# Optimization experiments

Hardware: AMD Instinct MI355X
Metric: run time of the kernel (lower is better)

## Reference

```python
import jax, jax.numpy as jnp
import numpy as np

B, D, H, L = 131072, 128, 128, 4
LN_EPS = 1e-5


def _layernorm(x, gamma, beta):
    mu = jnp.mean(x, axis=-1, keepdims=True)
    var = jnp.mean(jnp.square(x - mu), axis=-1, keepdims=True)
    return (x - mu) * jax.lax.rsqrt(var + LN_EPS) * gamma + beta


def setup_inputs() -> dict:
    key = jax.random.key(0)
    ks = jax.random.split(key, 12)
    t = jax.random.uniform(ks[0], (1,), dtype=jnp.float32)
    p = jax.random.normal(ks[1], (B, D), dtype=jnp.float32)
    w = jax.random.normal(ks[2], (B, D), dtype=jnp.float32)
    # VectorField parameters (torch default inits approximated with scaled normals)
    W_in = jax.random.normal(ks[3], (H, D), dtype=jnp.float32) * (1.0 / np.sqrt(D))
    b_in = jax.random.normal(ks[4], (H,), dtype=jnp.float32) * 0.01
    # FourierFeature buffers, scale=1.0 (hard-coded in VectorField)
    fw = jax.random.normal(ks[5], (L, H), dtype=jnp.float32) * 1.0
    fb = jax.random.uniform(ks[6], (L, H), dtype=jnp.float32) * 1.0
    gamma = jnp.ones((L, H), dtype=jnp.float32)
    beta = jnp.zeros((L, H), dtype=jnp.float32)
    Wl = jax.random.normal(ks[7], (L, H, H), dtype=jnp.float32) * (1.0 / np.sqrt(H))
    bl = jax.random.normal(ks[8], (L, H), dtype=jnp.float32) * 0.01
    W_out = jax.random.normal(ks[9], (D, H), dtype=jnp.float32) * (1.0 / np.sqrt(H))
    b_out = jax.random.normal(ks[10], (D,), dtype=jnp.float32) * 0.01
    return {"t": t, "p": p, "w": w, "W_in": W_in, "b_in": b_in, "fw": fw,
            "fb": fb, "gamma": gamma, "beta": beta, "Wl": Wl, "bl": bl,
            "W_out": W_out, "b_out": b_out}


def reference(t, p, w, W_in, b_in, fw, fb, gamma, beta, Wl, bl, W_out, b_out):
    # VectorField.forward: all ops act per-row, so batched vjp == vmapped per-sample vjp
    def vf(pp):  # pp: [B, D]
        h = pp @ W_in.T + b_in                      # [B, H]
        for i in range(L):
            h = h + jnp.sin(t * fw[i] + fb[i])      # time embedding, broadcast [H]
            h = jax.nn.softplus(h)
            h = _layernorm(h, gamma[i], beta[i])
            h = h @ Wl[i].T + bl[i]
        return h @ W_out.T + b_out                  # [B, D]

    dp, vjp_fn = jax.vjp(vf, p)
    dw = -vjp_fn(w)[0]
    return dp, dw
```

## Files before the change

kernel.cpp:

```cpp
#include <hip/hip_runtime.h>

typedef unsigned short u16;
typedef unsigned int   u32;
typedef __attribute__((ext_vector_type(8))) short bf16x8;
typedef __attribute__((ext_vector_type(4))) float f32x4;

#define NB 131072
#define LN_EPS 1e-5f
#define EX_STRIDE 136

__device__ __forceinline__ u16 f2b(float f){
  union { __bf16 h; u16 u; } c; c.h = (__bf16)f; return c.u;
}
__device__ __forceinline__ float upk(u32 pr, int hi){
  union { u32 u; float f; } c; c.u = hi ? (pr & 0xFFFF0000u) : (pr << 16); return c.f;
}
__device__ __forceinline__ float rowsum16(float x){
  x += __shfl_xor(x, 1);
  x += __shfl_xor(x, 2);
  x += __shfl_xor(x, 4);
  x += __shfl_xor(x, 8);
  return x;
}
__device__ __forceinline__ bf16x8 cvt8(const float* __restrict__ s){
  f32x4 x0 = *(const f32x4*)s;
  f32x4 x1 = *(const f32x4*)(s + 4);
  bf16x8 r;
  r[0]=(short)f2b(x0[0]); r[1]=(short)f2b(x0[1]);
  r[2]=(short)f2b(x0[2]); r[3]=(short)f2b(x0[3]);
  r[4]=(short)f2b(x1[0]); r[5]=(short)f2b(x1[1]);
  r[6]=(short)f2b(x1[2]); r[7]=(short)f2b(x1[3]);
  return r;
}

__device__ __forceinline__ void glds16(const u16* g, u16* l){
  __builtin_amdgcn_global_load_lds(
      (const __attribute__((address_space(1))) void*)g,
      (__attribute__((address_space(3))) void*)l, 16, 0, 0);
}
__device__ __forceinline__ void stageB(const u16* __restrict__ packB, int m,
                                       u16* __restrict__ bst, int wave, int lane){
  const u16* src = packB + m*16384 + wave*512 + lane*8;
  u16*       dst = bst   + wave*512;
  #pragma unroll
  for (int k = 0; k < 8; k++)
    glds16(src + k*2048, dst + k*2048);
}

__device__ __forceinline__ void gemm16(const bf16x8 a[4], const u16* __restrict__ Blds,
                                       int lane, f32x4 C[8]){
  const bf16x8* Bf = (const bf16x8*)Blds;
  #pragma unroll
  for (int nt = 0; nt < 8; nt++){
    f32x4 c = {0.f, 0.f, 0.f, 0.f};
    #pragma unroll
    for (int kt = 0; kt < 4; kt++){
      bf16x8 b = Bf[(nt*4 + kt)*64 + lane];
      c = __builtin_amdgcn_mfma_f32_16x16x32_bf16(a[kt], b, c, 0, 0, 0);
    }
    C[nt] = c;
  }
}

__global__ void prep_kernel(const float* __restrict__ t,   const float* __restrict__ W_in,
                            const float* __restrict__ b_in,const float* __restrict__ fw,
                            const float* __restrict__ fb,  const float* __restrict__ gamma,
                            const float* __restrict__ beta,const float* __restrict__ Wl,
                            const float* __restrict__ bl,  const float* __restrict__ W_out,
                            const float* __restrict__ b_out,
                            u16* __restrict__ packB, float* __restrict__ vecs)
{
  int bid = blockIdx.x, tid = threadIdx.x;
  if (bid < 768){
    int e    = bid*256 + tid;
    int m    = e >> 14;
    int r    = e & 16383;
    int fi   = r >> 9;
    int lane = (r >> 3) & 63;
    int j    = r & 7;
    int nt = fi >> 2, kt = fi & 3;
    int k = kt*32 + (lane >> 4)*8 + j;
    int n = nt*16 + (lane & 15);
    const float* src; bool tr;
    if      (m == 0){ src = W_in;              tr = true;  }
    else if (m <= 4){ src = Wl + (m-1)*16384;  tr = true;  }
    else if (m == 5){ src = W_out;             tr = true;  }
    else if (m == 6){ src = W_out;             tr = false; }
    else if (m <=10){ src = Wl + (m-7)*16384;  tr = false; }
    else            { src = W_in;              tr = false; }
    packB[e] = f2b(tr ? src[n*128 + k] : src[k*128 + n]);
  } else {
    int idx = (bid - 768)*256 + tid;
    float tv = t[0];
    float v;
    if      (idx <  512) v = sinf(tv * fw[idx] + fb[idx]);
    else if (idx <  640) v = b_in[idx - 512];
    else if (idx < 1152) v = bl[idx - 640];
    else if (idx < 1664) v = gamma[idx - 1152];
    else if (idx < 2176) v = beta[idx - 1664];
    else                 v = b_out[idx - 2176];
    vecs[idx] = v;
  }
}

__global__ __launch_bounds__(256, 3)
void fused_vf(const float* __restrict__ p, const float* __restrict__ w,
              const u16* __restrict__ packB, const float* __restrict__ vecs,
              float* __restrict__ dp_out, float* __restrict__ dw_out)
{
  __shared__ __align__(16) u16  exch[4 * 16 * EX_STRIDE];
  __shared__ __align__(16) u16  bstage[16384];

  const int tid  = threadIdx.x;
  const int wave = tid >> 6, lane = tid & 63;
  const int l15  = lane & 15, quad = lane >> 4;
  u16* ex = exch + wave * 16 * EX_STRIDE;

  stageB(packB, 0, bstage, wave, lane);
  const float* sS    = vecs;
  const float* sBin  = vecs + 512;
  const float* sBl   = vecs + 640;
  const float* sGam  = vecs + 1152;
  const float* sBet  = vecs + 1664;
  const float* sBout = vecs + 2176;

  const long rowBase = (long)blockIdx.x * 64 + wave * 16;

  u32   sp_ck[4][8][2];
  float mus[4][4];
  float invs[4][4];

  bf16x8 a[4];
  f32x4  C[8];

  {
    const float* pr = p + (size_t)(rowBase + l15)*128 + quad*8;
    #pragma unroll
    for (int kt = 0; kt < 4; kt++) a[kt] = cvt8(pr + kt*32);
  }
  __syncthreads();
  gemm16(a, bstage, lane, C);
  #pragma unroll
  for (int nt = 0; nt < 8; nt++){
    float bv = sBin[nt*16 + l15];
    #pragma unroll
    for (int r = 0; r < 4; r++) C[nt][r] += bv;
  }

  #pragma unroll
  for (int i = 0; i < 4; i++){
    __syncthreads();
    stageB(packB, 1+i, bstage, wave, lane);
    float sum[4] = {0,0,0,0}, ssq[4] = {0,0,0,0};
    #pragma unroll
    for (int nt = 0; nt < 8; nt++){
      float se = sS[i*128 + nt*16 + l15];
      #pragma unroll
      for (int r = 0; r < 4; r++){
        float x  = C[nt][r] + se;
        float e  = __expf(-fabsf(x));
        float li = __logf(1.0f + e);
        float sp = fmaxf(x, 0.0f) + li;
        u16 sb = f2b(sp);
        if (r & 1) sp_ck[i][nt][r>>1] |= ((u32)sb) << 16; else sp_ck[i][nt][r>>1] = sb;
        sum[r] += sp; ssq[r] += sp*sp;
        C[nt][r] = sp;
      }
    }
    float mu[4], inv[4];
    #pragma unroll
    for (int r = 0; r < 4; r++){
      float m1 = rowsum16(sum[r]) * (1.0f/128.0f);
      float m2 = rowsum16(ssq[r]) * (1.0f/128.0f);
      float var = m2 - m1*m1;
      mu[r] = m1; inv[r] = rsqrtf(fmaxf(var, 0.0f) + LN_EPS);
      mus[i][r] = m1; invs[i][r] = inv[r];
    }
    #pragma unroll
    for (int nt = 0; nt < 8; nt++){
      float g_ = sGam[i*128 + nt*16 + l15];
      float b_ = sBet[i*128 + nt*16 + l15];
      #pragma unroll
      for (int r = 0; r < 4; r++){
        float xh = (C[nt][r] - mu[r]) * inv[r];
        float v = xh * g_ + b_;
        ex[(quad*4 + r)*EX_STRIDE + nt*16 + l15] = f2b(v);
      }
    }
    __syncthreads();
    {
      const u16* rp = ex + l15*EX_STRIDE + quad*8;
      #pragma unroll
      for (int kt = 0; kt < 4; kt++) a[kt] = *(const bf16x8*)(rp + kt*32);
    }
    gemm16(a, bstage, lane, C);
    #pragma unroll
    for (int nt = 0; nt < 8; nt++){
      float bv = sBl[i*128 + nt*16 + l15];
      #pragma unroll
      for (int r = 0; r < 4; r++) C[nt][r] += bv;
    }
  }

  __syncthreads();
  stageB(packB, 5, bstage, wave, lane);
  #pragma unroll
  for (int nt = 0; nt < 8; nt++)
    #pragma unroll
    for (int r = 0; r < 4; r++)
      ex[(quad*4 + r)*EX_STRIDE + nt*16 + l15] = f2b(C[nt][r]);
  __syncthreads();
  {
    const u16* rp = ex + l15*EX_STRIDE + quad*8;
    #pragma unroll
    for (int kt = 0; kt < 4; kt++) a[kt] = *(const bf16x8*)(rp + kt*32);
  }
  gemm16(a, bstage, lane, C);
  {
    float* gp = dp_out + (size_t)rowBase*128;
    #pragma unroll
    for (int nt = 0; nt < 8; nt++){
      float bv = sBout[nt*16 + l15];
      #pragma unroll
      for (int r = 0; r < 4; r++)
        gp[(size_t)(quad*4 + r)*128 + nt*16 + l15] = C[nt][r] + bv;
    }
  }

  __syncthreads();
  stageB(packB, 6, bstage, wave, lane);
  {
    const float* wr = w + (size_t)(rowBase + l15)*128 + quad*8;
    #pragma unroll
    for (int kt = 0; kt < 4; kt++) a[kt] = cvt8(wr + kt*32);
  }
  __syncthreads();
  gemm16(a, bstage, lane, C);
  __syncthreads();
  stageB(packB, 10, bstage, wave, lane);

  #pragma unroll
  for (int ii = 0; ii < 4; ii++){
    const int i = 3 - ii;
    #pragma unroll
    for (int nt = 0; nt < 8; nt++)
      #pragma unroll
      for (int r = 0; r < 4; r++)
        ex[(quad*4 + r)*EX_STRIDE + nt*16 + l15] = f2b(C[nt][r]);
    __syncthreads();
    {
      const u16* rp = ex + l15*EX_STRIDE + quad*8;
      #pragma unroll
      for (int kt = 0; kt < 4; kt++) a[kt] = *(const bf16x8*)(rp + kt*32);
    }
    gemm16(a, bstage, lane, C);
    __syncthreads();
    stageB(packB, (ii < 3) ? (7 + (2 - ii)) : 11, bstage, wave, lane);
    float s1[4] = {0,0,0,0}, s2[4] = {0,0,0,0};
    #pragma unroll
    for (int nt = 0; nt < 8; nt++){
      float g_ = sGam[i*128 + nt*16 + l15];
      #pragma unroll
      for (int r = 0; r < 4; r++){
        float sp = upk(sp_ck[i][nt][r>>1], r & 1);
        float xh = (sp - mus[i][r]) * invs[i][r];
        float gx = C[nt][r] * g_;
        s1[r] += gx; s2[r] += gx * xh;
        C[nt][r] = gx;
      }
    }
    float m1[4], m2[4];
    #pragma unroll
    for (int r = 0; r < 4; r++){
      m1[r] = rowsum16(s1[r]) * (1.0f/128.0f);
      m2[r] = rowsum16(s2[r]) * (1.0f/128.0f);
    }
    #pragma unroll
    for (int nt = 0; nt < 8; nt++)
      #pragma unroll
      for (int r = 0; r < 4; r++){
        float sp = upk(sp_ck[i][nt][r>>1], r & 1);
        float xh = (sp - mus[i][r]) * invs[i][r];
        float sg = 1.0f - __expf(-sp);
        float gu = invs[i][r] * (C[nt][r] - m1[r] - xh * m2[r]);
        C[nt][r] = gu * sg;
      }
  }

  #pragma unroll
  for (int nt = 0; nt < 8; nt++)
    #pragma unroll
    for (int r = 0; r < 4; r++)
      ex[(quad*4 + r)*EX_STRIDE + nt*16 + l15] = f2b(C[nt][r]);
  __syncthreads();
  {
    const u16* rp = ex + l15*EX_STRIDE + quad*8;
    #pragma unroll
    for (int kt = 0; kt < 4; kt++) a[kt] = *(const bf16x8*)(rp + kt*32);
  }
  gemm16(a, bstage, lane, C);
  {
    float* gp = dw_out + (size_t)rowBase*128;
    #pragma unroll
    for (int nt = 0; nt < 8; nt++)
      #pragma unroll
      for (int r = 0; r < 4; r++)
        gp[(size_t)(quad*4 + r)*128 + nt*16 + l15] = -C[nt][r];
  }
}

extern "C" void kernel_launch(void* const* d_in, const int* in_sizes, int n_in,
                              void* d_out, int out_size, void* d_ws, size_t ws_size,
                              hipStream_t stream)
{
  const float* t     = (const float*)d_in[0];
  const float* p     = (const float*)d_in[1];
  const float* w     = (const float*)d_in[2];
  const float* W_in  = (const float*)d_in[3];
  const float* b_in  = (const float*)d_in[4];
  const float* fw    = (const float*)d_in[5];
  const float* fb    = (const float*)d_in[6];
  const float* gamma = (const float*)d_in[7];
  const float* beta  = (const float*)d_in[8];
  const float* Wl    = (const float*)d_in[9];
  const float* bl    = (const float*)d_in[10];
  const float* W_out = (const float*)d_in[11];
  const float* b_out = (const float*)d_in[12];

  u16*   packB = (u16*)d_ws;
  float* vecs  = (float*)((char*)d_ws + 12*16384*2);

  prep_kernel<<<777, 256, 0, stream>>>(t, W_in, b_in, fw, fb, gamma, beta,
                                       Wl, bl, W_out, b_out, packB, vecs);

  float* dp = (float*)d_out;
  float* dw = (float*)d_out + (size_t)NB * 128;
  fused_vf<<<NB/64, 256, 0, stream>>>(p, w, packB, vecs, dp, dw);
}
```

Before: 401.3 us.

## Fold LayerNorm affine into weights and recompute LN stats in backward

Gamma is folded into the packed forward and backward weight matrices, and beta into a precomputed effective bias (bl + Wl·beta). This drops the per-element affine work in the forward LN. The backward pass no longer keeps mean and inverse-std in registers; it recomputes them from the stored bf16 softplus values, which lowers register pressure. Time-embedding and layer-bias vectors are staged into LDS. The cost is extra row reductions in the backward pass, and LN statistics now come from bf16-rounded values, which may shift accuracy slightly.

```diff
diff --git a/kernel.cpp b/kernel.cpp
--- a/kernel.cpp
+++ b/kernel.cpp
@@ -88,18 +88,24 @@
     else if (m == 6){ src = W_out;             tr = false; }
     else if (m <=10){ src = Wl + (m-7)*16384;  tr = false; }
     else            { src = W_in;              tr = false; }
-    packB[e] = f2b(tr ? src[n*128 + k] : src[k*128 + n]);
+    float v = tr ? src[n*128 + k] : src[k*128 + n];
+    if      (m >= 1 && m <= 4)  v *= gamma[(m-1)*128 + k];
+    else if (m >= 7 && m <= 10) v *= gamma[(m-7)*128 + n];
+    packB[e] = f2b(v);
+  } else if (bid < 770){
+    int idx = (bid - 768)*256 + tid;
+    vecs[idx] = sinf(t[0] * fw[idx] + fb[idx]);
+  } else if (bid < 772){
+    int gid = (bid - 770)*256 + tid;
+    int i = gid >> 7, o = gid & 127;
+    const float* Wr = Wl + i*16384 + o*128;
+    const float* be = beta + i*128;
+    float acc = bl[gid];
+    for (int k2 = 0; k2 < 128; k2++) acc += be[k2] * Wr[k2];
+    vecs[512 + gid] = acc;
   } else {
-    int idx = (bid - 768)*256 + tid;
-    float tv = t[0];
-    float v;
-    if      (idx <  512) v = sinf(tv * fw[idx] + fb[idx]);
-    else if (idx <  640) v = b_in[idx - 512];
-    else if (idx < 1152) v = bl[idx - 640];
-    else if (idx < 1664) v = gamma[idx - 1152];
-    else if (idx < 2176) v = beta[idx - 1664];
-    else                 v = b_out[idx - 2176];
-    vecs[idx] = v;
+    if (tid < 128) vecs[1024 + tid]        = b_in[tid];
+    else           vecs[1152 + (tid-128)]  = b_out[tid-128];
   }
 }
 
@@ -110,6 +116,7 @@
 {
   __shared__ __align__(16) u16  exch[4 * 16 * EX_STRIDE];
   __shared__ __align__(16) u16  bstage[16384];
+  __shared__ float sv[1024];
 
   const int tid  = threadIdx.x;
   const int wave = tid >> 6, lane = tid & 63;
@@ -117,18 +124,15 @@
   u16* ex = exch + wave * 16 * EX_STRIDE;
 
   stageB(packB, 0, bstage, wave, lane);
-  const float* sS    = vecs;
-  const float* sBin  = vecs + 512;
-  const float* sBl   = vecs + 640;
-  const float* sGam  = vecs + 1152;
-  const float* sBet  = vecs + 1664;
-  const float* sBout = vecs + 2176;
+  for (int idx = tid; idx < 1024; idx += 256) sv[idx] = vecs[idx];
+  const float* sS   = sv;
+  const float* sBl  = sv + 512;
+  const float* gBin  = vecs + 1024;
+  const float* gBout = vecs + 1152;
 
   const long rowBase = (long)blockIdx.x * 64 + wave * 16;
 
   u32   sp_ck[4][8][2];
-  float mus[4][4];
-  float invs[4][4];
 
   bf16x8 a[4];
   f32x4  C[8];
@@ -142,7 +146,7 @@
   gemm16(a, bstage, lane, C);
   #pragma unroll
   for (int nt = 0; nt < 8; nt++){
-    float bv = sBin[nt*16 + l15];
+    float bv = gBin[nt*16 + l15];
     #pragma unroll
     for (int r = 0; r < 4; r++) C[nt][r] += bv;
   }
@@ -174,19 +178,14 @@
       float m2 = rowsum16(ssq[r]) * (1.0f/128.0f);
       float var = m2 - m1*m1;
       mu[r] = m1; inv[r] = rsqrtf(fmaxf(var, 0.0f) + LN_EPS);
-      mus[i][r] = m1; invs[i][r] = inv[r];
-    }
-    #pragma unroll
-    for (int nt = 0; nt < 8; nt++){
-      float g_ = sGam[i*128 + nt*16 + l15];
-      float b_ = sBet[i*128 + nt*16 + l15];
+    }
+    #pragma unroll
+    for (int nt = 0; nt < 8; nt++)
       #pragma unroll
       for (int r = 0; r < 4; r++){
         float xh = (C[nt][r] - mu[r]) * inv[r];
-        float v = xh * g_ + b_;
-        ex[(quad*4 + r)*EX_STRIDE + nt*16 + l15] = f2b(v);
+        ex[(quad*4 + r)*EX_STRIDE + nt*16 + l15] = f2b(xh);
       }
-    }
     __syncthreads();
     {
       const u16* rp = ex + l15*EX_STRIDE + quad*8;
@@ -220,7 +219,7 @@
     float* gp = dp_out + (size_t)rowBase*128;
     #pragma unroll
     for (int nt = 0; nt < 8; nt++){
-      float bv = sBout[nt*16 + l15];
+      float bv = gBout[nt*16 + l15];
       #pragma unroll
       for (int r = 0; r < 4; r++)
         gp[(size_t)(quad*4 + r)*128 + nt*16 + l15] = C[nt][r] + bv;
@@ -256,33 +255,37 @@
     gemm16(a, bstage, lane, C);
     __syncthreads();
     stageB(packB, (ii < 3) ? (7 + (2 - ii)) : 11, bstage, wave, lane);
-    float s1[4] = {0,0,0,0}, s2[4] = {0,0,0,0};
-    #pragma unroll
-    for (int nt = 0; nt < 8; nt++){
-      float g_ = sGam[i*128 + nt*16 + l15];
+    float ssp[4] = {0,0,0,0}, ss2[4] = {0,0,0,0};
+    float s1[4]  = {0,0,0,0}, sgs[4] = {0,0,0,0};
+    #pragma unroll
+    for (int nt = 0; nt < 8; nt++)
       #pragma unroll
       for (int r = 0; r < 4; r++){
         float sp = upk(sp_ck[i][nt][r>>1], r & 1);
-        float xh = (sp - mus[i][r]) * invs[i][r];
-        float gx = C[nt][r] * g_;
-        s1[r] += gx; s2[r] += gx * xh;
-        C[nt][r] = gx;
+        float gx = C[nt][r];
+        ssp[r] += sp; ss2[r] += sp*sp;
+        s1[r]  += gx; sgs[r] += gx*sp;
       }
-    }
-    float m1[4], m2[4];
+    float mu[4], inv[4], m1[4], m2[4];
     #pragma unroll
     for (int r = 0; r < 4; r++){
-      m1[r] = rowsum16(s1[r]) * (1.0f/128.0f);
-      m2[r] = rowsum16(s2[r]) * (1.0f/128.0f);
+      float sm  = rowsum16(ssp[r]) * (1.0f/128.0f);
+      float sq  = rowsum16(ss2[r]) * (1.0f/128.0f);
+      float var = sq - sm*sm;
+      float iv  = rsqrtf(fmaxf(var, 0.0f) + LN_EPS);
+      float g1  = rowsum16(s1[r])  * (1.0f/128.0f);
+      float ggs = rowsum16(sgs[r]) * (1.0f/128.0f);
+      mu[r] = sm; inv[r] = iv; m1[r] = g1;
+      m2[r] = iv * (ggs - sm*g1);
     }
     #pragma unroll
     for (int nt = 0; nt < 8; nt++)
       #pragma unroll
       for (int r = 0; r < 4; r++){
         float sp = upk(sp_ck[i][nt][r>>1], r & 1);
-        float xh = (sp - mus[i][r]) * invs[i][r];
+        float xh = (sp - mu[r]) * inv[r];
         float sg = 1.0f - __expf(-sp);
-        float gu = invs[i][r] * (C[nt][r] - m1[r] - xh * m2[r]);
+        float gu = inv[r] * (C[nt][r] - m1[r] - xh * m2[r]);
         C[nt][r] = gu * sg;
       }
   }
@@ -330,7 +333,7 @@
   u16*   packB = (u16*)d_ws;
   float* vecs  = (float*)((char*)d_ws + 12*16384*2);
 
-  prep_kernel<<<777, 256, 0, stream>>>(t, W_in, b_in, fw, fb, gamma, beta,
+  prep_kernel<<<773, 256, 0, stream>>>(t, W_in, b_in, fw, fb, gamma, beta,
                                        Wl, bl, W_out, b_out, packB, vecs);
 
   float* dp = (float*)d_out;
```

Result: slower. 411.2 us (+2.5%).
